# Performance work log

Hardware: AMD Instinct MI355X
Metric: run time of the kernel (lower is better)

## Reference

```python
import jax, jax.numpy as jnp
import numpy as np

N = 1024        # batch of tokens (module is per-token; we vmap via batched einsums)
IN = 1024       # in_features
H = 16          # num_heads
D = 64          # head_dim
BD = 512        # binary_dim
M = 8192        # num memories
OUT = H * D     # out_features
TEMP = 0.01
EPS = 1e-5


def setup_inputs() -> dict:
    key = jax.random.key(0)
    ks = jax.random.split(key, 8)
    return {
        "x": jax.random.normal(ks[0], (N, IN), jnp.float32),
        "Wq": jax.random.normal(ks[1], (OUT, IN), jnp.float32) / np.sqrt(IN).astype(np.float32),
        "bq_bias": jax.random.normal(ks[2], (OUT,), jnp.float32) * 0.01,
        "bin_proj": jax.random.normal(ks[3], (H, BD, D), jnp.float32),
        "bin_inv": jax.random.normal(ks[4], (H, D, BD), jnp.float32) / np.float32(BD),
        # binary memory codes in {-1, +1}
        "weight_matrix": jnp.sign(jax.random.normal(ks[5], (H, M, BD), jnp.float32)),
        "ln_w": jnp.ones((OUT,), jnp.float32),
        "ln_b": jnp.zeros((OUT,), jnp.float32),
    }


def reference(x, Wq, bq_bias, bin_proj, bin_inv, weight_matrix, ln_w, ln_b):
    # query projection: [N, OUT] -> [N, H, D], L2-normalize per head
    q = (x @ Wq.T + bq_bias).reshape(N, H, D)
    q = q / jnp.linalg.norm(q, axis=-1, keepdims=True)
    # sign-encode into binary space: [N, H, BD]
    code = jnp.sign(jnp.einsum('nhd,hbd->nhb', q, bin_proj))
    # cosine-transformed Hamming-similarity scores: [N, H, M]
    sim = jnp.einsum('nhb,hmb->nhm', code, weight_matrix) / np.float32(BD)
    scores = jnp.cos((np.float32(np.pi) / 2) * (1.0 - sim))
    attn = jax.nn.softmax(scores / np.float32(TEMP), axis=-1)
    # readout from binary memories, project back to real space
    out = jnp.einsum('nhm,hmb->nhb', attn, weight_matrix)
    out = jnp.einsum('nhb,hdb->nhd', out, bin_inv)
    out = out / jnp.linalg.norm(out, axis=-1, keepdims=True)
    out = out.reshape(N, OUT)
    # LayerNorm over out_features
    mu = jnp.mean(out, axis=-1, keepdims=True)
    var = jnp.var(out, axis=-1, keepdims=True)
    return (out - mu) / jnp.sqrt(var + np.float32(EPS)) * ln_w + ln_b
```

## Files before the change

### kernel.cpp

```cpp
#include <hip/hip_runtime.h>
#include <hip/hip_fp16.h>

#define NTOK 1024
#define INF  1024
#define NH   16
#define DH   64
#define BDIM 512
#define NMEM 8192
#define OUTF 1024
#define NWRD 16

typedef _Float16 f16x8 __attribute__((ext_vector_type(8)));
typedef float    f32x4 __attribute__((ext_vector_type(4)));
typedef int      i32x4 __attribute__((ext_vector_type(4)));

#define GLOAD16(G, L) __builtin_amdgcn_global_load_lds( \
    (const __attribute__((address_space(1))) unsigned int*)(G), \
    (__attribute__((address_space(3))) unsigned int*)(L), 16, 0, 0)

__device__ inline float score2(float s) {
  return 144.2695040889f * __sinf(s * 0.0030679615757712823f);
}

__global__ __launch_bounds__(256) void k_qgemm(const float* __restrict__ x,
    const float* __restrict__ Wq, const float* __restrict__ bq, float* __restrict__ q) {
  __shared__ float As[64][17];
  __shared__ float Bs[64][17];
  const int tx = threadIdx.x & 15, ty = threadIdx.x >> 4;
  const int n0 = blockIdx.y * 64, o0 = blockIdx.x * 64;
  const int r = threadIdx.x >> 2, c4 = (threadIdx.x & 3) * 4;
  float acc[4][4] = {};
  for (int k0 = 0; k0 < INF; k0 += 16) {
    float4 av = *(const float4*)&x[(size_t)(n0 + r) * INF + k0 + c4];
    float4 bv = *(const float4*)&Wq[(size_t)(o0 + r) * INF + k0 + c4];
    __syncthreads();
    As[r][c4+0] = av.x; As[r][c4+1] = av.y; As[r][c4+2] = av.z; As[r][c4+3] = av.w;
    Bs[r][c4+0] = bv.x; Bs[r][c4+1] = bv.y; Bs[r][c4+2] = bv.z; Bs[r][c4+3] = bv.w;
    __syncthreads();
    #pragma unroll
    for (int kk = 0; kk < 16; ++kk) {
      float a[4], b[4];
      #pragma unroll
      for (int i = 0; i < 4; ++i) a[i] = As[ty*4+i][kk];
      #pragma unroll
      for (int j = 0; j < 4; ++j) b[j] = Bs[tx*4+j][kk];
      #pragma unroll
      for (int i = 0; i < 4; ++i)
        #pragma unroll
        for (int j = 0; j < 4; ++j) acc[i][j] += a[i] * b[j];
    }
  }
  #pragma unroll
  for (int i = 0; i < 4; ++i) {
    const int row = n0 + ty*4 + i;
    #pragma unroll
    for (int j = 0; j < 4; ++j) {
      const int col = o0 + tx*4 + j;
      q[(size_t)row * OUTF + col] = acc[i][j] + bq[col];
    }
  }
}

__global__ __launch_bounds__(256) void k_code(const float* __restrict__ q,
    const float* __restrict__ bp, signed char* __restrict__ code_i8) {
  const int h = blockIdx.y, n0 = blockIdx.x * 16;
  __shared__ float ql[16][68];
  const int t = threadIdx.x;
  {
    const int r = t >> 4, c = (t & 15) * 4;
    float4 v = *(const float4*)&q[(size_t)(n0 + r) * OUTF + h * 64 + c];
    ql[r][c] = v.x; ql[r][c+1] = v.y; ql[r][c+2] = v.z; ql[r][c+3] = v.w;
  }
  __syncthreads();
  #pragma unroll
  for (int bb = 0; bb < 512; bb += 256) {
    const int b = bb + t;
    float bpv[64];
    const float4* src = (const float4*)&bp[((size_t)h * BDIM + b) * 64];
    #pragma unroll
    for (int j = 0; j < 16; ++j) {
      float4 v = src[j];
      bpv[j*4] = v.x; bpv[j*4+1] = v.y; bpv[j*4+2] = v.z; bpv[j*4+3] = v.w;
    }
    for (int n = 0; n < 16; ++n) {
      float dot = 0.f;
      #pragma unroll
      for (int d = 0; d < 64; ++d) dot += bpv[d] * ql[n][d];
      code_i8[((size_t)h * NTOK + n0 + n) * BDIM + b] = dot > 0.f ? 1 : -1;
    }
  }
}

__global__ __launch_bounds__(256) void k_packw(const float* __restrict__ w,
    unsigned* __restrict__ wp, signed char* __restrict__ w_i8) {
  const int row  = blockIdx.x * 4 + (threadIdx.x >> 6);
  const int lane = threadIdx.x & 63;
  const float* src = w + (size_t)row * BDIM;
  unsigned my = 0;
  #pragma unroll
  for (int kk = 0; kk < 8; ++kk) {
    float v = src[kk * 64 + lane];
    w_i8[(size_t)row * BDIM + kk * 64 + lane] = v > 0.f ? 1 : -1;
    unsigned long long m = __ballot(v > 0.f);
    if ((lane >> 1) == kk) my = (lane & 1) ? (unsigned)(m >> 32) : (unsigned)m;
  }
  if (lane < 16) wp[(size_t)row * NWRD + lane] = my;
}

__global__ __launch_bounds__(256) void k_binT(const float* __restrict__ binv,
                                              float* __restrict__ bT) {
  const int h = blockIdx.y, b0 = blockIdx.x * 64;
  __shared__ float tl[64][65];
  const int t = threadIdx.x;
  #pragma unroll
  for (int i = 0; i < 4; ++i) {
    int fi = t + 256 * i;
    int d = fi >> 4, b = (fi & 15) * 4;
    float4 v = *(const float4*)&binv[((size_t)h * DH + d) * BDIM + b0 + b];
    tl[d][b] = v.x; tl[d][b+1] = v.y; tl[d][b+2] = v.z; tl[d][b+3] = v.w;
  }
  __syncthreads();
  #pragma unroll
  for (int i = 0; i < 4; ++i) {
    int fo = t + 256 * i;
    int bb = fo >> 4, dd = (fo & 15) * 4;
    float4 v = { tl[dd][bb], tl[dd+1][bb], tl[dd+2][bb], tl[dd+3][bb] };
    *(float4*)&bT[((size_t)h * BDIM + b0 + bb) * DH + dd] = v;
  }
}

__global__ __launch_bounds__(256) void k_wt(const unsigned* __restrict__ wp,
    unsigned short* __restrict__ wt, int h0) {
  const int hg = blockIdx.z, h = h0 + hg;
  const int b0 = blockIdx.y * 64, m0 = blockIdx.x * 256;
  __shared__ unsigned bits[256][2];
  const int t = threadIdx.x;
  const unsigned* src = wp + (size_t)(h * NMEM + m0 + t) * NWRD + (b0 >> 5);
  bits[t][0] = src[0]; bits[t][1] = src[1];
  __syncthreads();
  const int b = t >> 2, ms = (t & 3) * 64;
  const int wd = b >> 5, sh = b & 31;
  const int bx7 = b & 7;
  unsigned short* dst = wt + ((size_t)hg * BDIM + b0 + b) * NMEM + m0 + ms;
  #pragma unroll
  for (int g = 0; g < 8; ++g) {
    const int pg = g ^ bx7;
    const int j = ms + g * 8;
    ushort4 v0, v1;
    v0.x = ((bits[j+0][wd] >> sh) & 1) ? 0x3C00 : 0xBC00;
    v0.y = ((bits[j+1][wd] >> sh) & 1) ? 0x3C00 : 0xBC00;
    v0.z = ((bits[j+2][wd] >> sh) & 1) ? 0x3C00 : 0xBC00;
    v0.w = ((bits[j+3][wd] >> sh) & 1) ? 0x3C00 : 0xBC00;
    v1.x = ((bits[j+4][wd] >> sh) & 1) ? 0x3C00 : 0xBC00;
    v1.y = ((bits[j+5][wd] >> sh) & 1) ? 0x3C00 : 0xBC00;
    v1.z = ((bits[j+6][wd] >> sh) & 1) ? 0x3C00 : 0xBC00;
    v1.w = ((bits[j+7][wd] >> sh) & 1) ? 0x3C00 : 0xBC00;
    *(ushort4*)&dst[pg * 8]     = v0;
    *(ushort4*)&dst[pg * 8 + 4] = v1;
  }
}

__global__ __launch_bounds__(512, 2) void k_sim(const signed char* __restrict__ code_i8,
    const signed char* __restrict__ w_i8, short* __restrict__ simb,
    int* __restrict__ rowmax, int h0, int gmask, int gshift) {
  const int bid = (int)blockIdx.x;
  const int hg = bid & gmask, h = h0 + hg;
  const int n0 = (bid >> gshift) * 64;
  const int t = threadIdx.x, lane = t & 63, wid = t >> 6;
  __shared__ int smaxl[64];
  if (t < 64) smaxl[t] = -(1 << 30);
  i32x4 afrag[4][8];
  #pragma unroll
  for (int fi = 0; fi < 4; ++fi)
    #pragma unroll
    for (int kk = 0; kk < 8; ++kk)
      afrag[fi][kk] = *(const i32x4*)(code_i8 +
          ((size_t)h * NTOK + n0 + fi * 16 + (lane & 15)) * BDIM +
          kk * 64 + (lane >> 4) * 16);
  __syncthreads();
  int vmax[4][4];
  #pragma unroll
  for (int fi = 0; fi < 4; ++fi)
    #pragma unroll
    for (int j = 0; j < 4; ++j) vmax[fi][j] = -(1 << 30);
  const signed char* bbase0 = w_i8 + (size_t)h * NMEM * BDIM +
                              (lane & 15) * BDIM + (lane >> 4) * 16;
  for (int i = 0; i < 32; ++i) {
    const int m0 = (i * 8 + wid) * 32;
    const signed char* bb = bbase0 + (size_t)m0 * BDIM;
    i32x4 acc[4][2] = {};
    #pragma unroll
    for (int kk = 0; kk < 8; ++kk) {
      i32x4 b0 = *(const i32x4*)(bb + kk * 64);
      i32x4 b1 = *(const i32x4*)(bb + 16 * BDIM + kk * 64);
      #pragma unroll
      for (int fi = 0; fi < 4; ++fi) {
        acc[fi][0] = __builtin_amdgcn_mfma_i32_16x16x64_i8(afrag[fi][kk], b0, acc[fi][0], 0, 0, 0);
        acc[fi][1] = __builtin_amdgcn_mfma_i32_16x16x64_i8(afrag[fi][kk], b1, acc[fi][1], 0, 0, 0);
      }
    }
    #pragma unroll
    for (int fi = 0; fi < 4; ++fi)
      #pragma unroll
      for (int j = 0; j < 4; ++j) {
        const int row = n0 + fi * 16 + (lane >> 4) * 4 + j;
        short* dst = simb + ((size_t)hg * NTOK + row) * NMEM + m0 + (lane & 15);
        const int v0 = acc[fi][0][j], v1 = acc[fi][1][j];
        dst[0]  = (short)v0;
        dst[16] = (short)v1;
        vmax[fi][j] = max(vmax[fi][j], max(v0, v1));
      }
  }
  #pragma unroll
  for (int fi = 0; fi < 4; ++fi)
    #pragma unroll
    for (int j = 0; j < 4; ++j) {
      int v = vmax[fi][j];
      #pragma unroll
      for (int s = 1; s < 16; s <<= 1) v = max(v, __shfl_xor(v, s));
      if ((lane & 15) == 0)
        atomicMax(&smaxl[fi * 16 + (lane >> 4) * 4 + j], v);
    }
  __syncthreads();
  if (t < 64) rowmax[(size_t)hg * NTOK + n0 + t] = smaxl[t];
}

__global__ __launch_bounds__(512, 2) void k_stageF(const short* __restrict__ simb,
    const int* __restrict__ rowmax, const unsigned short* __restrict__ wt,
    float* __restrict__ o1t, int gmask, int gshift) {
  __shared__ _Float16 Al[128][64];
  __shared__ _Float16 Bl[128][64];
  const int wg = (int)blockIdx.x;
  const int hg = wg & gmask;
  const int rest = wg >> gshift;
  const int nt = rest & 7, bt = rest >> 3;
  const int n0 = nt * 128, b0 = bt * 128;
  const int t = threadIdx.x;
  const int lane = t & 63, wid = t >> 6;
  const int wm = wid >> 2, wn = wid & 3;
  f32x4 acc[4][2];
  #pragma unroll
  for (int i = 0; i < 4; ++i)
    #pragma unroll
    for (int j = 0; j < 2; ++j) acc[i][j] = (f32x4){0.f, 0.f, 0.f, 0.f};

  const int rA0 = 16 * wid + (lane >> 3);
  const short* ag0 = simb + ((size_t)hg * NTOK + n0 + rA0) * NMEM + (lane & 7) * 8;
  const float sm0 = score2((float)rowmax[(size_t)hg * NTOK + n0 + rA0]);
  const float sm1 = score2((float)rowmax[(size_t)hg * NTOK + n0 + rA0 + 8]);
  const int awp = ((lane & 7) ^ ((lane >> 3) & 7)) * 8;
  const unsigned short* bg = wt + ((size_t)hg * BDIM + b0 + 16 * wid + (lane >> 3)) * NMEM + (lane & 7) * 8;
  _Float16* bl0 = &Bl[16 * wid][0];

  uint4 sA0 = *(const uint4*)(ag0);
  uint4 sA1 = *(const uint4*)(ag0 + 8 * NMEM);

  for (int k0 = 0; k0 < NMEM; k0 += 64) {
    f16x8 p0, p1;
    const short* s0p = (const short*)&sA0;
    const short* s1p = (const short*)&sA1;
    #pragma unroll
    for (int e = 0; e < 8; ++e) {
      p0[e] = (_Float16)exp2f(score2((float)s0p[e]) - sm0);
      p1[e] = (_Float16)exp2f(score2((float)s1p[e]) - sm1);
    }
    __syncthreads();
    *(f16x8*)&Al[rA0][awp]     = p0;
    *(f16x8*)&Al[rA0 + 8][awp] = p1;
    GLOAD16(bg + k0,            bl0);
    GLOAD16(bg + k0 + 8 * NMEM, bl0 + 8 * 64);
    __syncthreads();
    if (k0 + 64 < NMEM) {
      sA0 = *(const uint4*)(ag0 + k0 + 64);
      sA1 = *(const uint4*)(ag0 + k0 + 64 + 8 * NMEM);
    }
    #pragma unroll
    for (int kk = 0; kk < 64; kk += 32) {
      const int phys = (((kk >> 3) + (lane >> 4)) ^ (lane & 7)) * 8;
      f16x8 af[4], bf[2];
      #pragma unroll
      for (int fm = 0; fm < 4; ++fm)
        af[fm] = *(const f16x8*)&Al[wm*64 + fm*16 + (lane & 15)][phys];
      #pragma unroll
      for (int fn = 0; fn < 2; ++fn)
        bf[fn] = *(const f16x8*)&Bl[wn*32 + fn*16 + (lane & 15)][phys];
      #pragma unroll
      for (int fm = 0; fm < 4; ++fm)
        #pragma unroll
        for (int fn = 0; fn < 2; ++fn)
          acc[fm][fn] = __builtin_amdgcn_mfma_f32_16x16x32_f16(af[fm], bf[fn], acc[fm][fn], 0, 0, 0);
    }
  }
  #pragma unroll
  for (int fm = 0; fm < 4; ++fm) {
    const int rowb = n0 + wm*64 + fm*16 + (lane >> 4) * 4;
    #pragma unroll
    for (int fn = 0; fn < 2; ++fn) {
      const int col = b0 + wn*32 + fn*16 + (lane & 15);
      *(f32x4*)&o1t[((size_t)hg * BDIM + col) * NTOK + rowb] = acc[fm][fn];
    }
  }
}

__global__ __launch_bounds__(256) void k_proj(const float* __restrict__ o1t,
    const float* __restrict__ bT, float* __restrict__ o2, int h0) {
  const int hg = blockIdx.y, h = h0 + hg;
  const int n0 = blockIdx.x * 64;
  __shared__ float bl[128][68];
  __shared__ float ol[128][68];
  __shared__ float outl[64][68];
  __shared__ float nrm[64];
  const int t = threadIdx.x;
  const int tx = t & 15, ty = t >> 4;
  float acc[4][4] = {};
  for (int c = 0; c < 4; ++c) {
    const int bb0 = c * 128;
    __syncthreads();
    #pragma unroll
    for (int i = 0; i < 8; ++i) {
      int fi = t + 256 * i;
      int rr = fi >> 4, cc = (fi & 15) * 4;
      *(float4*)&bl[rr][cc] = *(const float4*)&bT[((size_t)h * BDIM + bb0 + rr) * DH + cc];
      *(float4*)&ol[rr][cc] = *(const float4*)&o1t[((size_t)hg * BDIM + bb0 + rr) * NTOK + n0 + cc];
    }
    __syncthreads();
    for (int bb = 0; bb < 128; ++bb) {
      float4 bd = *(const float4*)&bl[bb][tx * 4];
      float4 on = *(const float4*)&ol[bb][ty * 4];
      float ai[4] = {on.x, on.y, on.z, on.w};
      float bj[4] = {bd.x, bd.y, bd.z, bd.w};
      #pragma unroll
      for (int i = 0; i < 4; ++i)
        #pragma unroll
        for (int j = 0; j < 4; ++j) acc[i][j] += ai[i] * bj[j];
    }
  }
  __syncthreads();
  #pragma unroll
  for (int i = 0; i < 4; ++i)
    #pragma unroll
    for (int j = 0; j < 4; ++j) outl[ty*4 + i][tx*4 + j] = acc[i][j];
  __syncthreads();
  if (t < 64) {
    float s = 0.f;
    #pragma unroll
    for (int d = 0; d < 64; ++d) { float v = outl[t][d]; s += v * v; }
    nrm[t] = 1.f / sqrtf(s);
  }
  __syncthreads();
  {
    const int n = t >> 2, dg = (t & 3) * 16;
    #pragma unroll
    for (int j = 0; j < 16; ++j)
      o2[(size_t)(n0 + n) * OUTF + h * 64 + dg + j] = outl[n][dg + j] * nrm[n];
  }
}

__global__ __launch_bounds__(256) void k_ln(const float* __restrict__ o2,
    const float* __restrict__ lnw, const float* __restrict__ lnb, float* __restrict__ out) {
  const int n = blockIdx.x, t = threadIdx.x;
  __shared__ float red[4];
  float4 v = *(const float4*)&o2[(size_t)n * OUTF + t * 4];
  float s = v.x + v.y + v.z + v.w;
  const int lane = t & 63, wid = t >> 6;
  #pragma unroll
  for (int off = 32; off; off >>= 1) s += __shfl_down(s, off);
  if (lane == 0) red[wid] = s;
  __syncthreads();
  const float mu = (red[0] + red[1] + red[2] + red[3]) * (1.f / 1024.f);
  float4 d = {v.x - mu, v.y - mu, v.z - mu, v.w - mu};
  float s2 = d.x*d.x + d.y*d.y + d.z*d.z + d.w*d.w;
  #pragma unroll
  for (int off = 32; off; off >>= 1) s2 += __shfl_down(s2, off);
  __syncthreads();
  if (lane == 0) red[wid] = s2;
  __syncthreads();
  const float var = (red[0] + red[1] + red[2] + red[3]) * (1.f / 1024.f);
  const float inv = 1.f / sqrtf(var + 1e-5f);
  float4 w = *(const float4*)&lnw[t * 4];
  float4 b = *(const float4*)&lnb[t * 4];
  float4 o = { d.x*inv*w.x + b.x, d.y*inv*w.y + b.y,
               d.z*inv*w.z + b.z, d.w*inv*w.w + b.w };
  *(float4*)&out[(size_t)n * OUTF + t * 4] = o;
}

extern "C" void kernel_launch(void* const* d_in, const int* in_sizes, int n_in,
                              void* d_out, int out_size, void* d_ws, size_t ws_size,
                              hipStream_t stream) {
  (void)in_sizes; (void)n_in; (void)out_size;
  const float* x    = (const float*)d_in[0];
  const float* Wq   = (const float*)d_in[1];
  const float* bq   = (const float*)d_in[2];
  const float* bp   = (const float*)d_in[3];
  const float* binv = (const float*)d_in[4];
  const float* wm   = (const float*)d_in[5];
  const float* lnw  = (const float*)d_in[6];
  const float* lnb  = (const float*)d_in[7];
  float* outp = (float*)d_out;

  char* ws = (char*)d_ws;
  size_t off = 0;
  auto carve = [&](size_t bytes) -> char* {
    char* p = ws + off;
    off += (bytes + 255) & ~(size_t)255;
    return p;
  };
  float*       q       = (float*)      carve((size_t)NTOK * OUTF * 4);
  signed char* code_i8 = (signed char*)carve((size_t)NH * NTOK * BDIM);
  unsigned*    wpk     = (unsigned*)   carve((size_t)NH * NMEM * NWRD * 4);
  signed char* w_i8    = (signed char*)carve((size_t)NH * NMEM * BDIM);
  float*       bT      = (float*)      carve((size_t)NH * BDIM * DH * 4);
  float*       o2      = (float*)      carve((size_t)NTOK * OUTF * 4);
  const size_t fixed = off;
  const size_t per = ((size_t)BDIM * NMEM * 2 + 256)
                   + ((size_t)NTOK * NMEM * 2 + 256)
                   + ((size_t)BDIM * NTOK * 4 + 256)
                   + ((size_t)NTOK * 4 + 256);
  int G = 16;
  while (G > 1 && fixed + (size_t)G * per > ws_size) G >>= 1;
  unsigned short* wt   = (unsigned short*)carve((size_t)G * BDIM * NMEM * 2);
  short*          simb = (short*)         carve((size_t)G * NTOK * NMEM * 2);
  float*          o1t  = (float*)         carve((size_t)G * BDIM * NTOK * 4);
  int*            rmax = (int*)           carve((size_t)G * NTOK * 4);
  const int gshift = __builtin_ctz(G);

  k_qgemm<<<dim3(16, 16), 256, 0, stream>>>(x, Wq, bq, q);
  k_code <<<dim3(64, 16), 256, 0, stream>>>(q, bp, code_i8);
  k_packw<<<dim3(NH * NMEM / 4), 256, 0, stream>>>(wm, wpk, w_i8);
  k_binT <<<dim3(8, 16), 256, 0, stream>>>(binv, bT);
  for (int h0 = 0; h0 < NH; h0 += G) {
    k_wt    <<<dim3(32, 8, G), 256, 0, stream>>>(wpk, wt, h0);
    k_sim   <<<dim3(16 * G),   512, 0, stream>>>(code_i8, w_i8, simb, rmax, h0, G - 1, gshift);
    k_stageF<<<dim3(32 * G),   512, 0, stream>>>(simb, rmax, wt, o1t, G - 1, gshift);
    k_proj  <<<dim3(16, G),    256, 0, stream>>>(o1t, bT, o2, h0);
  }
  k_ln<<<dim3(NTOK), 256, 0, stream>>>(o2, lnw, lnb, outp);
}
```

Baseline: 756.1 us.

## Move softmax exponentiation into k_sim epilogue with score lookup table

k_sim now uses its block-local row max to convert the int16 similarity rows in place into fp16 exp2 probabilities. The score function comes from a 513-entry shared-memory lookup table. The probabilities are written with an XOR swizzle so k_stageF can copy them straight into LDS with global_load_lds, and the rowmax buffer goes away. This removes the repeated per-tile exp/sin work that each of the 4 b-tiles in k_stageF redid. The cost is an extra read-modify-write pass over the simb buffer inside k_sim, which relies on that block's own global writes being visible to it after the barrier.

```diff
diff --git a/kernel.cpp b/kernel.cpp
--- a/kernel.cpp
+++ b/kernel.cpp
@@ -162,13 +162,16 @@
 
 __global__ __launch_bounds__(512, 2) void k_sim(const signed char* __restrict__ code_i8,
     const signed char* __restrict__ w_i8, short* __restrict__ simb,
-    int* __restrict__ rowmax, int h0, int gmask, int gshift) {
+    int h0, int gmask, int gshift) {
   const int bid = (int)blockIdx.x;
   const int hg = bid & gmask, h = h0 + hg;
   const int n0 = (bid >> gshift) * 64;
   const int t = threadIdx.x, lane = t & 63, wid = t >> 6;
   __shared__ int smaxl[64];
+  __shared__ float sct[513];
   if (t < 64) smaxl[t] = -(1 << 30);
+  for (int p = t; p < 513; p += 512)
+    sct[p] = score2(2.f * (float)p - 512.f);
   i32x4 afrag[4][8];
   #pragma unroll
   for (int fi = 0; fi < 4; ++fi)
@@ -185,6 +188,7 @@
     for (int j = 0; j < 4; ++j) vmax[fi][j] = -(1 << 30);
   const signed char* bbase0 = w_i8 + (size_t)h * NMEM * BDIM +
                               (lane & 15) * BDIM + (lane >> 4) * 16;
+  short* srow = simb + ((size_t)hg * NTOK + n0) * NMEM;
   for (int i = 0; i < 32; ++i) {
     const int m0 = (i * 8 + wid) * 32;
     const signed char* bb = bbase0 + (size_t)m0 * BDIM;
@@ -203,8 +207,8 @@
     for (int fi = 0; fi < 4; ++fi)
       #pragma unroll
       for (int j = 0; j < 4; ++j) {
-        const int row = n0 + fi * 16 + (lane >> 4) * 4 + j;
-        short* dst = simb + ((size_t)hg * NTOK + row) * NMEM + m0 + (lane & 15);
+        const int row = fi * 16 + (lane >> 4) * 4 + j;
+        short* dst = srow + (size_t)row * NMEM + m0 + (lane & 15);
         const int v0 = acc[fi][0][j], v1 = acc[fi][1][j];
         dst[0]  = (short)v0;
         dst[16] = (short)v1;
@@ -222,12 +226,38 @@
         atomicMax(&smaxl[fi * 16 + (lane >> 4) * 4 + j], v);
     }
   __syncthreads();
-  if (t < 64) rowmax[(size_t)hg * NTOK + n0 + t] = smaxl[t];
-}
-
-__global__ __launch_bounds__(512, 2) void k_stageF(const short* __restrict__ simb,
-    const int* __restrict__ rowmax, const unsigned short* __restrict__ wt,
-    float* __restrict__ o1t, int gmask, int gshift) {
+  unsigned short* arow = (unsigned short*)srow;
+  for (int it = 0; it < 16; ++it) {
+    const int gw = it * 512 + t;
+    const int row = gw >> 7, win = gw & 127;
+    const float sm2 = sct[(smaxl[row] + 512) >> 1];
+    const short* sp = srow + (size_t)row * NMEM + win * 64;
+    uint4 sv[8];
+    #pragma unroll
+    for (int c = 0; c < 8; ++c) sv[c] = *(const uint4*)(sp + c * 8);
+    const int rx = row & 7;
+    unsigned short* dp = arow + (size_t)row * NMEM + win * 64;
+    #pragma unroll
+    for (int c = 0; c < 8; ++c) {
+      unsigned ov[4];
+      #pragma unroll
+      for (int k = 0; k < 4; ++k) {
+        const unsigned w2 = (&sv[c].x)[k];
+        const int lo = (int)(short)(w2 & 0xffffu);
+        const int hi = (int)(short)(w2 >> 16);
+        float p0 = exp2f(sct[(lo + 512) >> 1] - sm2);
+        float p1 = exp2f(sct[(hi + 512) >> 1] - sm2);
+        ov[k] = (unsigned)__half_as_ushort(__float2half(p0))
+              | ((unsigned)__half_as_ushort(__float2half(p1)) << 16);
+      }
+      *(uint4*)(dp + (c ^ rx) * 8) = make_uint4(ov[0], ov[1], ov[2], ov[3]);
+    }
+  }
+}
+
+__global__ __launch_bounds__(512, 2) void k_stageF(const unsigned short* __restrict__ attn,
+    const unsigned short* __restrict__ wt, float* __restrict__ o1t,
+    int gmask, int gshift) {
   __shared__ _Float16 Al[128][64];
   __shared__ _Float16 Bl[128][64];
   const int wg = (int)blockIdx.x;
@@ -244,36 +274,18 @@
     #pragma unroll
     for (int j = 0; j < 2; ++j) acc[i][j] = (f32x4){0.f, 0.f, 0.f, 0.f};
 
-  const int rA0 = 16 * wid + (lane >> 3);
-  const short* ag0 = simb + ((size_t)hg * NTOK + n0 + rA0) * NMEM + (lane & 7) * 8;
-  const float sm0 = score2((float)rowmax[(size_t)hg * NTOK + n0 + rA0]);
-  const float sm1 = score2((float)rowmax[(size_t)hg * NTOK + n0 + rA0 + 8]);
-  const int awp = ((lane & 7) ^ ((lane >> 3) & 7)) * 8;
-  const unsigned short* bg = wt + ((size_t)hg * BDIM + b0 + 16 * wid + (lane >> 3)) * NMEM + (lane & 7) * 8;
+  const unsigned short* ag = attn + ((size_t)hg * NTOK + n0 + 16*wid + (lane >> 3)) * NMEM + (lane & 7) * 8;
+  const unsigned short* bg = wt   + ((size_t)hg * BDIM + b0 + 16*wid + (lane >> 3)) * NMEM + (lane & 7) * 8;
+  _Float16* al0 = &Al[16 * wid][0];
   _Float16* bl0 = &Bl[16 * wid][0];
 
-  uint4 sA0 = *(const uint4*)(ag0);
-  uint4 sA1 = *(const uint4*)(ag0 + 8 * NMEM);
-
   for (int k0 = 0; k0 < NMEM; k0 += 64) {
-    f16x8 p0, p1;
-    const short* s0p = (const short*)&sA0;
-    const short* s1p = (const short*)&sA1;
-    #pragma unroll
-    for (int e = 0; e < 8; ++e) {
-      p0[e] = (_Float16)exp2f(score2((float)s0p[e]) - sm0);
-      p1[e] = (_Float16)exp2f(score2((float)s1p[e]) - sm1);
-    }
-    __syncthreads();
-    *(f16x8*)&Al[rA0][awp]     = p0;
-    *(f16x8*)&Al[rA0 + 8][awp] = p1;
+    __syncthreads();
+    GLOAD16(ag + k0,            al0);
+    GLOAD16(ag + k0 + 8 * NMEM, al0 + 8 * 64);
     GLOAD16(bg + k0,            bl0);
     GLOAD16(bg + k0 + 8 * NMEM, bl0 + 8 * 64);
     __syncthreads();
-    if (k0 + 64 < NMEM) {
-      sA0 = *(const uint4*)(ag0 + k0 + 64);
-      sA1 = *(const uint4*)(ag0 + k0 + 64 + 8 * NMEM);
-    }
     #pragma unroll
     for (int kk = 0; kk < 64; kk += 32) {
       const int phys = (((kk >> 3) + (lane >> 4)) ^ (lane & 7)) * 8;
@@ -414,14 +426,12 @@
   const size_t fixed = off;
   const size_t per = ((size_t)BDIM * NMEM * 2 + 256)
                    + ((size_t)NTOK * NMEM * 2 + 256)
-                   + ((size_t)BDIM * NTOK * 4 + 256)
-                   + ((size_t)NTOK * 4 + 256);
+                   + ((size_t)BDIM * NTOK * 4 + 256);
   int G = 16;
   while (G > 1 && fixed + (size_t)G * per > ws_size) G >>= 1;
   unsigned short* wt   = (unsigned short*)carve((size_t)G * BDIM * NMEM * 2);
   short*          simb = (short*)         carve((size_t)G * NTOK * NMEM * 2);
   float*          o1t  = (float*)         carve((size_t)G * BDIM * NTOK * 4);
-  int*            rmax = (int*)           carve((size_t)G * NTOK * 4);
   const int gshift = __builtin_ctz(G);
 
   k_qgemm<<<dim3(16, 16), 256, 0, stream>>>(x, Wq, bq, q);
@@ -430,8 +440,8 @@
   k_binT <<<dim3(8, 16), 256, 0, stream>>>(binv, bT);
   for (int h0 = 0; h0 < NH; h0 += G) {
     k_wt    <<<dim3(32, 8, G), 256, 0, stream>>>(wpk, wt, h0);
-    k_sim   <<<dim3(16 * G),   512, 0, stream>>>(code_i8, w_i8, simb, rmax, h0, G - 1, gshift);
-    k_stageF<<<dim3(32 * G),   512, 0, stream>>>(simb, rmax, wt, o1t, G - 1, gshift);
+    k_sim   <<<dim3(16 * G),   512, 0, stream>>>(code_i8, w_i8, simb, h0, G - 1, gshift);
+    k_stageF<<<dim3(32 * G),   512, 0, stream>>>((const unsigned short*)simb, wt, o1t, G - 1, gshift);
     k_proj  <<<dim3(16, G),    256, 0, stream>>>(o1t, bT, o2, h0);
   }
   k_ln<<<dim3(NTOK), 256, 0, stream>>>(o2, lnw, lnb, outp);
```

Measured after the change: 783.3 us. +3.6%, slower.
